# Optimization experiments

Measured on AMD Instinct MI355X. Metric: run time of the kernel, lower is better.

The kernel has to match this reference:

```python
import jax, jax.numpy as jnp
import numpy as np

IN_C, OUT_C = 32, 32
M1 = M2 = M3 = 12
CFT_M1 = CFT_M2 = M1 // 4  # 3
L_SEG, M_CHEB = 8, 6


def cft2d(x, m1, m2, L, M):
    # Piecewise Chebyshev projection along H (L segments, M polys), rFFT along W.
    # x: [N, C, H, W] -> complex [N, C, m1, m2]
    N, C, H, W = x.shape
    seg = H // L
    t = jnp.linspace(-1.0, 1.0, seg)
    theta = jnp.arccos(jnp.clip(t, -1.0, 1.0))
    P = jnp.cos(jnp.arange(M)[:, None] * theta[None, :])  # [M, seg] Chebyshev T_k
    xs = x.reshape(N, C, L, seg, W)
    coef = jnp.einsum('nclsw,ms->nclmw', xs, P) / seg      # [N,C,L,M,W]
    coef = coef.reshape(N, C, L * M, W)[:, :, :m1, :]      # keep first m1 coeffs
    return jnp.fft.rfft(coef, axis=-1)[:, :, :, :m2]       # [N,C,m1,m2] complex


def setup_inputs() -> dict:
    key = jax.random.key(0)
    ks = jax.random.split(key, 16)
    B, H, W, D = 4, 64, 64, 64
    scale = 1.0 / (IN_C * OUT_C)
    wshape = (IN_C, OUT_C, M1, M2, M3)
    inp = {'x': jax.random.normal(ks[0], (B, IN_C, H, W, D), dtype=jnp.float32)}
    for i in range(4):
        inp[f'w{i+1}_re'] = scale * jax.random.uniform(ks[1 + 2 * i], wshape, dtype=jnp.float32)
        inp[f'w{i+1}_im'] = scale * jax.random.uniform(ks[2 + 2 * i], wshape, dtype=jnp.float32)
    cft_flat = IN_C * CFT_M1 * CFT_M2 * 2  # 576
    hidden = (IN_C + OUT_C) * 2            # 128
    inp['mlp_w1'] = 0.02 * jax.random.normal(ks[9], (cft_flat, hidden), dtype=jnp.float32)
    inp['mlp_b1'] = jnp.zeros((hidden,), dtype=jnp.float32)
    inp['mlp_w2'] = 0.02 * jax.random.normal(ks[10], (hidden, OUT_C), dtype=jnp.float32)
    inp['mlp_b2'] = jnp.zeros((OUT_C,), dtype=jnp.float32)
    inp['corr_scale'] = jnp.float32(0.1)
    return inp


def reference(x, w1_re, w1_im, w2_re, w2_im, w3_re, w3_im, w4_re, w4_im,
              mlp_w1, mlp_b1, mlp_w2, mlp_b2, corr_scale):
    B, C, H, W, D = x.shape
    O = mlp_w2.shape[1]
    x_ft = jnp.fft.rfftn(x, axes=(-3, -2, -1))  # [B,C,H,W,D//2+1] complex64

    def mix(xb, wre, wim):
        return jnp.einsum('bixyz,ioxyz->boxyz', xb, wre + 1j * wim)

    out_ft = jnp.zeros((B, O, H, W, D // 2 + 1), dtype=x_ft.dtype)
    out_ft = out_ft.at[:, :, :M1, :M2, :M3].set(mix(x_ft[:, :, :M1, :M2, :M3], w1_re, w1_im))
    out_ft = out_ft.at[:, :, -M1:, :M2, :M3].set(mix(x_ft[:, :, -M1:, :M2, :M3], w2_re, w2_im))
    out_ft = out_ft.at[:, :, :M1, -M2:, :M3].set(mix(x_ft[:, :, :M1, -M2:, :M3], w3_re, w3_im))
    out_ft = out_ft.at[:, :, -M1:, -M2:, :M3].set(mix(x_ft[:, :, -M1:, -M2:, :M3], w4_re, w4_im))
    x_fno = jnp.fft.irfftn(out_ft, s=(H, W, D), axes=(-3, -2, -1))

    # Chebyshev-Fourier correction branch over depth slices
    xs = jnp.transpose(x, (0, 4, 1, 2, 3)).reshape(B * D, C, H, W)
    cft = cft2d(xs, CFT_M1, CFT_M2, L_SEG, M_CHEB)                 # [B*D,C,3,3] complex
    cft_flat = jnp.stack([cft.real, cft.imag], axis=-1).reshape(B * D, -1)  # view_as_real order
    h = jax.nn.gelu(cft_flat @ mlp_w1 + mlp_b1, approximate=False)
    corr = h @ mlp_w2 + mlp_b2                                     # [B*D, O]
    corr = jnp.transpose(corr.reshape(B, D, O), (0, 2, 1))[:, :, None, None, :]  # [B,O,1,1,D]
    return x_fno + corr_scale * corr
```

## Files before the change

### kernel.cpp

```cpp
#include <hip/hip_runtime.h>
#include <math.h>


#define CMUL_STEP(t, u) do { float _nx = (t).x*(u).x - (t).y*(u).y; \
    (t).y = (t).x*(u).y + (t).y*(u).x; (t).x = _nx; } while (0)

constexpr float TW_C[64] = {
     1.000000000000000f,  0.995184726672197f,  0.980785280403230f,  0.956940335732209f,
     0.923879532511287f,  0.881921264348355f,  0.831469612302545f,  0.773010453362737f,
     0.707106781186548f,  0.634393284163645f,  0.555570233019602f,  0.471396736825998f,
     0.382683432365090f,  0.290284677254462f,  0.195090322016128f,  0.098017140329561f,
     0.000000000000000f, -0.098017140329561f, -0.195090322016128f, -0.290284677254462f,
    -0.382683432365090f, -0.471396736825998f, -0.555570233019602f, -0.634393284163645f,
    -0.707106781186548f, -0.773010453362737f, -0.831469612302545f, -0.881921264348355f,
    -0.923879532511287f, -0.956940335732209f, -0.980785280403230f, -0.995184726672197f,
    -1.000000000000000f, -0.995184726672197f, -0.980785280403230f, -0.956940335732209f,
    -0.923879532511287f, -0.881921264348355f, -0.831469612302545f, -0.773010453362737f,
    -0.707106781186548f, -0.634393284163645f, -0.555570233019602f, -0.471396736825998f,
    -0.382683432365090f, -0.290284677254462f, -0.195090322016128f, -0.098017140329561f,
     0.000000000000000f,  0.098017140329561f,  0.195090322016128f,  0.290284677254462f,
     0.382683432365090f,  0.471396736825998f,  0.555570233019602f,  0.634393284163645f,
     0.707106781186548f,  0.773010453362737f,  0.831469612302545f,  0.881921264348355f,
     0.923879532511287f,  0.956940335732209f,  0.980785280403230f,  0.995184726672197f
};
constexpr float twc(int m) { return TW_C[m & 63]; }
constexpr float tws(int m) { return TW_C[(m + 48) & 63]; }

static __device__ __forceinline__ void fill_tw(float2* tw, int tid, int nthr) {
    for (int m = tid; m < 64; m += nthr) {
        float s, c;
        sincosf((float)m * 0.09817477042468103f, &s, &c);
        tw[m] = make_float2(c, s);
    }
}

static __device__ __forceinline__ void ystage_pair(const float2* __restrict__ Ar,
                                                   const float2* __restrict__ Br,
                                                   int ap, float2& A, float2& Bc) {
    const float2 zw0 = Ar[0];
    const float2 zw32 = Ar[32];
    const float sg = (ap & 1) ? -1.f : 1.f;
    A.x = zw0.x + sg * zw32.x;  A.y = zw0.y + sg * zw32.y;
    Bc = A;
    float s_, c_;
    sincosf((float)ap * 0.09817477042468103f, &s_, &c_);
    const float2 u = make_float2(c_, s_);
    float2 t = u;
    {
        float2 za = Ar[1], zb = Br[1];
        float Ex = za.x + zb.x, Ey = za.y + zb.y;
        float Ox = za.x - zb.x, Oy = za.y - zb.y;
        A.x  += t.x * Ex + t.y * Oy;  A.y  += t.x * Ey - t.y * Ox;
        Bc.x += t.x * Ex - t.y * Oy;  Bc.y += t.x * Ey + t.y * Ox;
    }
    #pragma unroll
    for (int w = 2; w < 32; w += 2) {
        CMUL_STEP(t, u);
        const float4 a4 = *(const float4*)(Ar + w);
        const float4 b4 = *(const float4*)(Br + w);
        {
            float Ex = a4.x + b4.x, Ey = a4.y + b4.y;
            float Ox = a4.x - b4.x, Oy = a4.y - b4.y;
            A.x  += t.x * Ex + t.y * Oy;  A.y  += t.x * Ey - t.y * Ox;
            Bc.x += t.x * Ex - t.y * Oy;  Bc.y += t.x * Ey + t.y * Ox;
        }
        CMUL_STEP(t, u);
        {
            float Ex = a4.z + b4.z, Ey = a4.w + b4.w;
            float Ox = a4.z - b4.z, Oy = a4.w - b4.w;
            A.x  += t.x * Ex + t.y * Oy;  A.y  += t.x * Ey - t.y * Ox;
            Bc.x += t.x * Ex - t.y * Oy;  Bc.y += t.x * Ey + t.y * Ox;
        }
    }
}

template<int KZ0>
static __device__ __forceinline__ void zstage_wave(const float* __restrict__ row,
                                                   float2* __restrict__ zA,
                                                   float2* __restrict__ zB,
                                                   int w) {
    float a0x, a0y = 0.f, a1x, a1y = 0.f, a2x, a2y = 0.f;
#define ACCD(dd, xa, xb) do { \
    const float e_ = (xa) + (xb), o_ = (xa) - (xb); \
    a0x += e_ * twc((KZ0    ) * (dd));  a0y -= o_ * tws((KZ0    ) * (dd)); \
    a1x += e_ * twc((KZ0 + 1) * (dd));  a1y -= o_ * tws((KZ0 + 1) * (dd)); \
    a2x += e_ * twc((KZ0 + 2) * (dd));  a2y -= o_ * tws((KZ0 + 2) * (dd)); } while (0)
    float4 qa  = *(const float4*)(row + 0);
    float4 qm1 = *(const float4*)(row + 60);
    float4 qm0 = *(const float4*)(row + 56);
    const float x0v = qa.x;
    a0x = x0v; a1x = x0v; a2x = x0v;
    ACCD(1, qa.y, qm1.w);
    ACCD(2, qa.z, qm1.z);
    ACCD(3, qa.w, qm1.y);
    float mnext = qm1.x;
    qa = *(const float4*)(row + 4);
    ACCD(4, qa.x, mnext);
    ACCD(5, qa.y, qm0.w);
    ACCD(6, qa.z, qm0.z);
    ACCD(7, qa.w, qm0.y);
    mnext = qm0.x;
    qm0 = *(const float4*)(row + 52);
    qa  = *(const float4*)(row + 8);
    ACCD(8,  qa.x, mnext);
    ACCD(9,  qa.y, qm0.w);
    ACCD(10, qa.z, qm0.z);
    ACCD(11, qa.w, qm0.y);
    mnext = qm0.x;
    qm0 = *(const float4*)(row + 48);
    qa  = *(const float4*)(row + 12);
    ACCD(12, qa.x, mnext);
    ACCD(13, qa.y, qm0.w);
    ACCD(14, qa.z, qm0.z);
    ACCD(15, qa.w, qm0.y);
    mnext = qm0.x;
    qm0 = *(const float4*)(row + 44);
    qa  = *(const float4*)(row + 16);
    ACCD(16, qa.x, mnext);
    ACCD(17, qa.y, qm0.w);
    ACCD(18, qa.z, qm0.z);
    ACCD(19, qa.w, qm0.y);
    mnext = qm0.x;
    qm0 = *(const float4*)(row + 40);
    qa  = *(const float4*)(row + 20);
    ACCD(20, qa.x, mnext);
    ACCD(21, qa.y, qm0.w);
    ACCD(22, qa.z, qm0.z);
    ACCD(23, qa.w, qm0.y);
    mnext = qm0.x;
    qm0 = *(const float4*)(row + 36);
    qa  = *(const float4*)(row + 24);
    ACCD(24, qa.x, mnext);
    ACCD(25, qa.y, qm0.w);
    ACCD(26, qa.z, qm0.z);
    ACCD(27, qa.w, qm0.y);
    mnext = qm0.x;
    qm0 = *(const float4*)(row + 32);
    qa  = *(const float4*)(row + 28);
    ACCD(28, qa.x, mnext);
    ACCD(29, qa.y, qm0.w);
    ACCD(30, qa.z, qm0.z);
    ACCD(31, qa.w, qm0.y);
    const float x32v = qm0.x;
#undef ACCD
    const float s0 = ((KZ0     & 1)) ? -x32v : x32v;
    const float s1 = (((KZ0+1) & 1)) ? -x32v : x32v;
    a0x += s0; a1x += s1; a2x += s0;
    zA[(KZ0    ) * 66 + w] = make_float2(a0x, a0y);
    zA[(KZ0 + 1) * 66 + w] = make_float2(a1x, a1y);
    zA[(KZ0 + 2) * 66 + w] = make_float2(a2x, a2y);
    const int wm = 64 - w;
    zB[(KZ0    ) * 66 + wm] = make_float2(a0x, a0y);
    zB[(KZ0 + 1) * 66 + wm] = make_float2(a1x, a1y);
    zB[(KZ0 + 2) * 66 + wm] = make_float2(a2x, a2y);
}

__global__ __launch_bounds__(256) void k_fwd_zy(const float* __restrict__ x,
                                                float2* __restrict__ X2) {
    __shared__ __align__(16) float xt[64 * 68];
    __shared__ __align__(16) float2 zA[12 * 66];
    __shared__ __align__(16) float2 zB[12 * 66];
    const int tid = threadIdx.x;
    const int blk = blockIdx.x;
    const float4* xrow4 = (const float4*)(x + (size_t)blk * 4096);
    for (int r = 0; r < 4; ++r) {
        int i4 = r * 256 + tid;
        int w = i4 >> 4, d4 = (i4 & 15) << 2;
        *(float4*)&xt[w * 68 + d4] = xrow4[i4];
    }
    __syncthreads();
    {
        const int q = tid >> 6, w = tid & 63;
        const float* row = &xt[w * 68];
        switch (q) {
            case 0: zstage_wave<0>(row, zA, zB, w); break;
            case 1: zstage_wave<3>(row, zA, zB, w); break;
            case 2: zstage_wave<6>(row, zA, zB, w); break;
            default: zstage_wave<9>(row, zA, zB, w); break;
        }
    }
    __syncthreads();
    float2* xout = X2 + (size_t)blk * 288;
    if (tid < 156) {
        const int ap = tid / 12, kz = tid - (tid / 12) * 12;
        float2 A, Bc;
        ystage_pair(&zA[kz * 66], &zB[kz * 66], ap, A, Bc);
        if (ap <= 11) xout[ap * 12 + kz] = A;
        if (ap >= 1)  xout[(24 - ap) * 12 + kz] = Bc;
    }
}

__global__ __launch_bounds__(256) void k_fwd_x(const float2* __restrict__ X2,
                                               float2* __restrict__ X3) {
    __shared__ __align__(16) float2 s2A[12 * 66];
    __shared__ __align__(16) float2 s2B[12 * 66];
    const int tid = threadIdx.x;
    const int blk = blockIdx.x;
    const int ay = blk % 24, bc = blk / 24;
    const float2* src = X2 + (size_t)bc * (64 * 288) + ay * 12;
    for (int i4 = tid; i4 < 384; i4 += 256) {
        int hh = i4 / 6, c4 = i4 - hh * 6;
        float4 v = ((const float4*)(src + (size_t)hh * 288))[c4];
        int kz = 2 * c4;
        s2A[kz * 66 + hh]            = make_float2(v.x, v.y);
        s2A[(kz + 1) * 66 + hh]      = make_float2(v.z, v.w);
        s2B[kz * 66 + (64 - hh)]     = make_float2(v.x, v.y);
        s2B[(kz + 1) * 66 + (64 - hh)] = make_float2(v.z, v.w);
    }
    __syncthreads();
    float2* dst = X3 + (size_t)bc * 6912 + ay * 12;
    if (tid < 156) {
        const int ap = tid / 12, kz = tid - (tid / 12) * 12;
        float2 A, Bc;
        ystage_pair(&s2A[kz * 66], &s2B[kz * 66], ap, A, Bc);
        if (ap <= 11) dst[ap * 288 + kz] = A;
        if (ap >= 1)  dst[(24 - ap) * 288 + kz] = Bc;
    }
}

__global__ __launch_bounds__(384) void k_mix(const float2* __restrict__ X3,
                                             float2* __restrict__ F,
        const float* __restrict__ w1re, const float* __restrict__ w1im,
        const float* __restrict__ w2re, const float* __restrict__ w2im,
        const float* __restrict__ w3re, const float* __restrict__ w3im,
        const float* __restrict__ w4re, const float* __restrict__ w4im) {
    __shared__ float2 xs[128 * 12];
    const int tid = threadIdx.x;
    const int blk = blockIdx.x;
    const int ax = blk / 24, ay = blk % 24;
    const int cx = ax >= 12 ? 1 : 0, cy = ay >= 12 ? 1 : 0;
    const int m1 = ax - cx * 12, m2 = ay - cy * 12;
    const int sel = cx + cy * 2;
    const float* wre = sel == 0 ? w1re : sel == 1 ? w2re : sel == 2 ? w3re : w4re;
    const float* wim = sel == 0 ? w1im : sel == 1 ? w2im : sel == 2 ? w3im : w4im;
    const size_t moff = (size_t)ax * 288 + (size_t)ay * 12;
    for (int i = tid; i < 1536; i += 384) {
        int bi = i / 12, kz = i - bi * 12;
        xs[i] = X3[(size_t)bi * 6912 + moff + kz];
    }
    __syncthreads();
    const int o = tid / 12, kz = tid - (tid / 12) * 12;
    const int wbase = o * 1728 + m1 * 144 + m2 * 12 + kz;
    float2 A0 = make_float2(0.f, 0.f), A1 = A0, A2 = A0, A3 = A0;
    for (int i = 0; i < 32; ++i) {
        float wr = wre[i * 55296 + wbase];
        float wi = wim[i * 55296 + wbase];
        float2 x0 = xs[i * 12 + kz];
        float2 x1 = xs[(32 + i) * 12 + kz];
        float2 x2 = xs[(64 + i) * 12 + kz];
        float2 x3 = xs[(96 + i) * 12 + kz];
        A0.x += x0.x * wr - x0.y * wi; A0.y += x0.x * wi + x0.y * wr;
        A1.x += x1.x * wr - x1.y * wi; A1.y += x1.x * wi + x1.y * wr;
        A2.x += x2.x * wr - x2.y * wi; A2.y += x2.x * wi + x2.y * wr;
        A3.x += x3.x * wr - x3.y * wi; A3.y += x3.x * wi + x3.y * wr;
    }
    F[(size_t)(0 * 32 + o) * 6912 + moff + kz] = A0;
    F[(size_t)(1 * 32 + o) * 6912 + moff + kz] = A1;
    F[(size_t)(2 * 32 + o) * 6912 + moff + kz] = A2;
    F[(size_t)(3 * 32 + o) * 6912 + moff + kz] = A3;
}

__global__ __launch_bounds__(256) void k_inv_x(const float2* __restrict__ F,
                                               float2* __restrict__ Y1) {
    __shared__ __align__(16) float2 fs[24 * 12];
    __shared__ float2 tw[64];
    const int tid = threadIdx.x;
    const int blk = blockIdx.x;
    const int ay = blk % 24, bo = blk / 24;
    fill_tw(tw, tid, 256);
    const float2* src = F + (size_t)bo * 6912 + ay * 12;
    for (int i4 = tid; i4 < 144; i4 += 256) {
        int ax = i4 / 6, c4 = i4 - ax * 6;
        ((float4*)&fs[ax * 12])[c4] = ((const float4*)(src + (size_t)ax * 288))[c4];
    }
    __syncthreads();
    float2* dst = Y1 + (size_t)bo * (64 * 288) + ay * 12;
    for (int idx = tid; idx < 396; idx += 256) {
        int hp = idx / 12, kz = idx - (idx / 12) * 12;
        float2 f0  = fs[kz];
        float2 f12 = fs[12 * 12 + kz];
        float2 t12 = tw[(52 * hp) & 63];
        float2 A, Bc;
        A.x  = f0.x + f12.x * t12.x - f12.y * t12.y;
        A.y  = f0.y + f12.x * t12.y + f12.y * t12.x;
        Bc.x = f0.x + f12.x * t12.x + f12.y * t12.y;
        Bc.y = f0.y + f12.y * t12.x - f12.x * t12.y;
        const float2 u = tw[hp];
        float2 t = u;
        for (int a = 1; a <= 11; ++a) {
            float2 fa = fs[a * 12 + kz];
            float2 fb = fs[(24 - a) * 12 + kz];
            float Ex = fa.x + fb.x, Ey = fa.y + fb.y;
            float Ox = fa.x - fb.x, Oy = fa.y - fb.y;
            A.x  += t.x * Ex - t.y * Oy;  A.y  += t.x * Ey + t.y * Ox;
            Bc.x += t.x * Ex + t.y * Oy;  Bc.y += t.x * Ey - t.y * Ox;
            CMUL_STEP(t, u);
        }
        dst[hp * 288 + kz] = A;
        if (hp >= 1 && hp <= 31) dst[(64 - hp) * 288 + kz] = Bc;
    }
}

__global__ __launch_bounds__(256) void k_cft(const float* __restrict__ x,
                                             float* __restrict__ cft) {
    __shared__ float2 tw[64];
    __shared__ float red[3 * 64 * 18];
    const int tid = threadIdx.x;
    const int blk = blockIdx.x;
    const int d = tid & 63, q = tid >> 6;
    fill_tw(tw, tid, 256);
    __syncthreads();
    float aR[3][3] = {{0.f}}, aI[3][3] = {{0.f}};
    const float* xb = x + (size_t)blk * 262144;
    for (int wi = 0; wi < 16; ++wi) {
        const int w = q * 16 + wi;
        float c0 = 0.f, c1 = 0.f, c2 = 0.f;
        #pragma unroll
        for (int s = 0; s < 8; ++s) {
            float xv = xb[(size_t)(s * 64 + w) * 64 + d];
            float t = (2.0f * (float)s - 7.0f) * (1.0f / 7.0f);
            c0 += xv;
            c1 += xv * t;
            c2 += xv * (2.0f * t * t - 1.0f);
        }
        c0 *= 0.125f; c1 *= 0.125f; c2 *= 0.125f;
        #pragma unroll
        for (int f = 0; f < 3; ++f) {
            float2 t = tw[(f * w) & 63];
            aR[0][f] += c0 * t.x; aI[0][f] -= c0 * t.y;
            aR[1][f] += c1 * t.x; aI[1][f] -= c1 * t.y;
            aR[2][f] += c2 * t.x; aI[2][f] -= c2 * t.y;
        }
    }
    if (q > 0) {
        float* dst = &red[((q - 1) * 64 + d) * 18];
        #pragma unroll
        for (int k = 0; k < 3; ++k)
            #pragma unroll
            for (int f = 0; f < 3; ++f) {
                dst[k * 6 + f * 2]     = aR[k][f];
                dst[k * 6 + f * 2 + 1] = aI[k][f];
            }
    }
    __syncthreads();
    if (q == 0) {
        #pragma unroll
        for (int qq = 0; qq < 3; ++qq) {
            const float* sr = &red[(qq * 64 + d) * 18];
            #pragma unroll
            for (int k = 0; k < 3; ++k)
                #pragma unroll
                for (int f = 0; f < 3; ++f) {
                    aR[k][f] += sr[k * 6 + f * 2];
                    aI[k][f] += sr[k * 6 + f * 2 + 1];
                }
        }
        const int b = blk >> 5, c = blk & 31;
        float* dst = cft + (size_t)(b * 64 + d) * 576 + c * 18;
        #pragma unroll
        for (int k = 0; k < 3; ++k)
            #pragma unroll
            for (int f = 0; f < 3; ++f) {
                dst[k * 6 + f * 2]     = aR[k][f];
                dst[k * 6 + f * 2 + 1] = aI[k][f];
            }
    }
}

__global__ __launch_bounds__(128) void k_mlp(const float* __restrict__ cft,
                                             const float* __restrict__ w1,
                                             const float* __restrict__ b1,
                                             const float* __restrict__ w2,
                                             const float* __restrict__ b2,
                                             const float* __restrict__ cs,
                                             float* __restrict__ corr) {
    __shared__ float row[576];
    __shared__ float hbuf[128];
    const int n = blockIdx.x;
    const int tid = threadIdx.x;
    for (int i = tid; i < 576; i += 128) row[i] = cft[(size_t)n * 576 + i];
    __syncthreads();
    float acc = b1[tid];
    #pragma unroll 8
    for (int k = 0; k < 576; ++k) acc += row[k] * w1[k * 128 + tid];
    hbuf[tid] = 0.5f * acc * (1.0f + erff(acc * 0.70710678118654752f));
    __syncthreads();
    if (tid < 32) {
        float a2 = b2[tid];
        #pragma unroll 8
        for (int k = 0; k < 128; ++k) a2 += hbuf[k] * w2[k * 32 + tid];
        const int b = n >> 6, d = n & 63;
        corr[(b * 32 + tid) * 64 + d] = a2 * cs[0];
    }
}

__global__ __launch_bounds__(256) void k_inv_yz(const float2* __restrict__ Y1,
                                                const float* __restrict__ corr,
                                                float* __restrict__ out) {
    __shared__ __align__(16) float2 y1[288];
    __shared__ __align__(16) float2 y2[64 * 12];
    __shared__ float2 tw[64];
    __shared__ float corrl[64];
    const int tid = threadIdx.x;
    const int blk = blockIdx.x;
    const int bo = blk >> 6;
    fill_tw(tw, tid, 256);
    {
        const float4* src4 = (const float4*)(Y1 + (size_t)blk * 288);
        for (int i4 = tid; i4 < 144; i4 += 256) ((float4*)y1)[i4] = src4[i4];
    }
    if (tid < 64) corrl[tid] = corr[bo * 64 + tid];
    __syncthreads();
    {
        const int w = tid >> 2, kz0 = (tid & 3) * 3;
        float2 a0 = make_float2(0.f, 0.f), a1 = a0, a2 = a0;
        {
            float2 f0 = y1[kz0], f1 = y1[kz0 + 1], f2 = y1[kz0 + 2];
            a0.x += f0.x; a0.y += f0.y;
            a1.x += f1.x; a1.y += f1.y;
            a2.x += f2.x; a2.y += f2.y;
        }
        {
            float2 t = tw[(52 * w) & 63];
            float2 f0 = y1[144 + kz0], f1 = y1[144 + kz0 + 1], f2 = y1[144 + kz0 + 2];
            a0.x += f0.x * t.x - f0.y * t.y; a0.y += f0.x * t.y + f0.y * t.x;
            a1.x += f1.x * t.x - f1.y * t.y; a1.y += f1.x * t.y + f1.y * t.x;
            a2.x += f2.x * t.x - f2.y * t.y; a2.y += f2.x * t.y + f2.y * t.x;
        }
        const float2 u = tw[w];
        float2 t = u;
        for (int a = 1; a <= 11; ++a) {
            const float2* fa = &y1[a * 12 + kz0];
            const float2* fb = &y1[(24 - a) * 12 + kz0];
            float2 p0 = fa[0], p1 = fa[1], p2 = fa[2];
            float2 q0 = fb[0], q1 = fb[1], q2 = fb[2];
            float Ex, Ey, Ox, Oy;
            Ex = p0.x + q0.x; Ey = p0.y + q0.y; Ox = p0.x - q0.x; Oy = p0.y - q0.y;
            a0.x += t.x * Ex - t.y * Oy; a0.y += t.x * Ey + t.y * Ox;
            Ex = p1.x + q1.x; Ey = p1.y + q1.y; Ox = p1.x - q1.x; Oy = p1.y - q1.y;
            a1.x += t.x * Ex - t.y * Oy; a1.y += t.x * Ey + t.y * Ox;
            Ex = p2.x + q2.x; Ey = p2.y + q2.y; Ox = p2.x - q2.x; Oy = p2.y - q2.y;
            a2.x += t.x * Ex - t.y * Oy; a2.y += t.x * Ey + t.y * Ox;
            CMUL_STEP(t, u);
        }
        y2[w * 12 + kz0]     = a0;
        y2[w * 12 + kz0 + 1] = a1;
        y2[w * 12 + kz0 + 2] = a2;
    }
    float ctw[12], stw[12];
    const int d = tid & 63;
    #pragma unroll
    for (int kz = 0; kz < 12; ++kz) {
        float2 t = tw[(kz * d) & 63];
        float sc = (kz == 0 ? 1.0f : 2.0f) * (1.0f / 262144.0f);
        ctw[kz] = t.x * sc;
        stw[kz] = t.y * sc;
    }
    __syncthreads();
    const float cv = corrl[d];
    float* orow = out + (size_t)blk * 4096;
    const int wq = tid >> 6;
    for (int r = 0; r < 16; ++r) {
        int w = r * 4 + wq;
        const float4* yv = (const float4*)&y2[w * 12];
        float4 p0 = yv[0], p1 = yv[1], p2 = yv[2];
        float4 p3 = yv[3], p4 = yv[4], p5 = yv[5];
        float s = cv;
        s += p0.x * ctw[0]  - p0.y * stw[0];
        s += p0.z * ctw[1]  - p0.w * stw[1];
        s += p1.x * ctw[2]  - p1.y * stw[2];
        s += p1.z * ctw[3]  - p1.w * stw[3];
        s += p2.x * ctw[4]  - p2.y * stw[4];
        s += p2.z * ctw[5]  - p2.w * stw[5];
        s += p3.x * ctw[6]  - p3.y * stw[6];
        s += p3.z * ctw[7]  - p3.w * stw[7];
        s += p4.x * ctw[8]  - p4.y * stw[8];
        s += p4.z * ctw[9]  - p4.w * stw[9];
        s += p5.x * ctw[10] - p5.y * stw[10];
        s += p5.z * ctw[11] - p5.w * stw[11];
        orow[w * 64 + d] = s;
    }
}

extern "C" void kernel_launch(void* const* d_in, const int* in_sizes, int n_in,
                              void* d_out, int out_size, void* d_ws, size_t ws_size,
                              hipStream_t stream) {
    const float* x    = (const float*)d_in[0];
    const float* w1re = (const float*)d_in[1];
    const float* w1im = (const float*)d_in[2];
    const float* w2re = (const float*)d_in[3];
    const float* w2im = (const float*)d_in[4];
    const float* w3re = (const float*)d_in[5];
    const float* w3im = (const float*)d_in[6];
    const float* w4re = (const float*)d_in[7];
    const float* w4im = (const float*)d_in[8];
    const float* mw1  = (const float*)d_in[9];
    const float* mb1  = (const float*)d_in[10];
    const float* mw2  = (const float*)d_in[11];
    const float* mb2  = (const float*)d_in[12];
    const float* cs   = (const float*)d_in[13];
    float* out = (float*)d_out;

    char* ws = (char*)d_ws;
    float2* X2   = (float2*)(ws);
    float2* X3   = (float2*)(ws + 18874368);
    float2* F    = (float2*)(ws + 25952256);
    float*  cft  = (float*) (ws + 33030144);
    float*  corr = (float*) (ws + 33619968);
    float2* Y1   = X2;

    hipLaunchKernelGGL(k_fwd_zy, dim3(8192), dim3(256), 0, stream, x, X2);
    hipLaunchKernelGGL(k_fwd_x,  dim3(3072), dim3(256), 0, stream, X2, X3);
    hipLaunchKernelGGL(k_mix,    dim3(576),  dim3(384), 0, stream, X3, F,
                       w1re, w1im, w2re, w2im, w3re, w3im, w4re, w4im);
    hipLaunchKernelGGL(k_inv_x,  dim3(3072), dim3(256), 0, stream, F, Y1);
    hipLaunchKernelGGL(k_cft,    dim3(128),  dim3(256), 0, stream, x, cft);
    hipLaunchKernelGGL(k_mlp,    dim3(256),  dim3(128), 0, stream,
                       cft, mw1, mb1, mw2, mb2, cs, corr);
    hipLaunchKernelGGL(k_inv_yz, dim3(8192), dim3(256), 0, stream, Y1, corr, out);
}
```

Measured before the change: 479.7 us.

## Use one wave per block in z-stage FFT, loading rows into registers

The forward z/y stage now launches 64-thread blocks. Each thread loads its whole 64-element row straight into registers and computes all 12 z-modes itself, so the shared-memory staging of x and its barrier are gone. The y-stage work is looped over the single wave instead of being spread across 256 threads. This trades four-wave parallelism per block for fewer LDS round trips, at the cost of higher register pressure (64 loaded floats plus 24 accumulators) and more serial work per thread.

```diff
diff --git a/kernel.cpp b/kernel.cpp
--- a/kernel.cpp
+++ b/kernel.cpp
@@ -74,119 +74,57 @@
     }
 }
 
-template<int KZ0>
-static __device__ __forceinline__ void zstage_wave(const float* __restrict__ row,
-                                                   float2* __restrict__ zA,
-                                                   float2* __restrict__ zB,
-                                                   int w) {
-    float a0x, a0y = 0.f, a1x, a1y = 0.f, a2x, a2y = 0.f;
-#define ACCD(dd, xa, xb) do { \
-    const float e_ = (xa) + (xb), o_ = (xa) - (xb); \
-    a0x += e_ * twc((KZ0    ) * (dd));  a0y -= o_ * tws((KZ0    ) * (dd)); \
-    a1x += e_ * twc((KZ0 + 1) * (dd));  a1y -= o_ * tws((KZ0 + 1) * (dd)); \
-    a2x += e_ * twc((KZ0 + 2) * (dd));  a2y -= o_ * tws((KZ0 + 2) * (dd)); } while (0)
-    float4 qa  = *(const float4*)(row + 0);
-    float4 qm1 = *(const float4*)(row + 60);
-    float4 qm0 = *(const float4*)(row + 56);
-    const float x0v = qa.x;
-    a0x = x0v; a1x = x0v; a2x = x0v;
-    ACCD(1, qa.y, qm1.w);
-    ACCD(2, qa.z, qm1.z);
-    ACCD(3, qa.w, qm1.y);
-    float mnext = qm1.x;
-    qa = *(const float4*)(row + 4);
-    ACCD(4, qa.x, mnext);
-    ACCD(5, qa.y, qm0.w);
-    ACCD(6, qa.z, qm0.z);
-    ACCD(7, qa.w, qm0.y);
-    mnext = qm0.x;
-    qm0 = *(const float4*)(row + 52);
-    qa  = *(const float4*)(row + 8);
-    ACCD(8,  qa.x, mnext);
-    ACCD(9,  qa.y, qm0.w);
-    ACCD(10, qa.z, qm0.z);
-    ACCD(11, qa.w, qm0.y);
-    mnext = qm0.x;
-    qm0 = *(const float4*)(row + 48);
-    qa  = *(const float4*)(row + 12);
-    ACCD(12, qa.x, mnext);
-    ACCD(13, qa.y, qm0.w);
-    ACCD(14, qa.z, qm0.z);
-    ACCD(15, qa.w, qm0.y);
-    mnext = qm0.x;
-    qm0 = *(const float4*)(row + 44);
-    qa  = *(const float4*)(row + 16);
-    ACCD(16, qa.x, mnext);
-    ACCD(17, qa.y, qm0.w);
-    ACCD(18, qa.z, qm0.z);
-    ACCD(19, qa.w, qm0.y);
-    mnext = qm0.x;
-    qm0 = *(const float4*)(row + 40);
-    qa  = *(const float4*)(row + 20);
-    ACCD(20, qa.x, mnext);
-    ACCD(21, qa.y, qm0.w);
-    ACCD(22, qa.z, qm0.z);
-    ACCD(23, qa.w, qm0.y);
-    mnext = qm0.x;
-    qm0 = *(const float4*)(row + 36);
-    qa  = *(const float4*)(row + 24);
-    ACCD(24, qa.x, mnext);
-    ACCD(25, qa.y, qm0.w);
-    ACCD(26, qa.z, qm0.z);
-    ACCD(27, qa.w, qm0.y);
-    mnext = qm0.x;
-    qm0 = *(const float4*)(row + 32);
-    qa  = *(const float4*)(row + 28);
-    ACCD(28, qa.x, mnext);
-    ACCD(29, qa.y, qm0.w);
-    ACCD(30, qa.z, qm0.z);
-    ACCD(31, qa.w, qm0.y);
-    const float x32v = qm0.x;
-#undef ACCD
-    const float s0 = ((KZ0     & 1)) ? -x32v : x32v;
-    const float s1 = (((KZ0+1) & 1)) ? -x32v : x32v;
-    a0x += s0; a1x += s1; a2x += s0;
-    zA[(KZ0    ) * 66 + w] = make_float2(a0x, a0y);
-    zA[(KZ0 + 1) * 66 + w] = make_float2(a1x, a1y);
-    zA[(KZ0 + 2) * 66 + w] = make_float2(a2x, a2y);
-    const int wm = 64 - w;
-    zB[(KZ0    ) * 66 + wm] = make_float2(a0x, a0y);
-    zB[(KZ0 + 1) * 66 + wm] = make_float2(a1x, a1y);
-    zB[(KZ0 + 2) * 66 + wm] = make_float2(a2x, a2y);
-}
-
-__global__ __launch_bounds__(256) void k_fwd_zy(const float* __restrict__ x,
-                                                float2* __restrict__ X2) {
-    __shared__ __align__(16) float xt[64 * 68];
+__global__ __launch_bounds__(64) void k_fwd_zy(const float* __restrict__ x,
+                                               float2* __restrict__ X2) {
     __shared__ __align__(16) float2 zA[12 * 66];
     __shared__ __align__(16) float2 zB[12 * 66];
-    const int tid = threadIdx.x;
-    const int blk = blockIdx.x;
-    const float4* xrow4 = (const float4*)(x + (size_t)blk * 4096);
-    for (int r = 0; r < 4; ++r) {
-        int i4 = r * 256 + tid;
-        int w = i4 >> 4, d4 = (i4 & 15) << 2;
-        *(float4*)&xt[w * 68 + d4] = xrow4[i4];
-    }
-    __syncthreads();
+    const int w = threadIdx.x;
+    const int blk = blockIdx.x;
+    const float4* row4 = (const float4*)(x + (size_t)blk * 4096 + (size_t)w * 64);
+    float4 q[16];
+    #pragma unroll
+    for (int j = 0; j < 16; ++j) q[j] = row4[j];
+    float ax[12], ay[12];
     {
-        const int q = tid >> 6, w = tid & 63;
-        const float* row = &xt[w * 68];
-        switch (q) {
-            case 0: zstage_wave<0>(row, zA, zB, w); break;
-            case 1: zstage_wave<3>(row, zA, zB, w); break;
-            case 2: zstage_wave<6>(row, zA, zB, w); break;
-            default: zstage_wave<9>(row, zA, zB, w); break;
-        }
+        const float x0v = q[0].x, x32v = q[8].x;
+        #pragma unroll
+        for (int k = 0; k < 12; ++k) {
+            ax[k] = x0v + ((k & 1) ? -x32v : x32v);
+            ay[k] = 0.f;
+        }
+    }
+#define QE(dd) ((dd) & 3) == 0 ? q[(dd) >> 2].x : ((dd) & 3) == 1 ? q[(dd) >> 2].y : \
+               ((dd) & 3) == 2 ? q[(dd) >> 2].z : q[(dd) >> 2].w
+    #pragma unroll
+    for (int d = 1; d < 32; ++d) {
+        const float xa = QE(d);
+        const float xb = QE(64 - d);
+        const float e = xa + xb, o = xa - xb;
+        #pragma unroll
+        for (int k = 0; k < 12; ++k) {
+            ax[k] += e * twc(k * d);
+            ay[k] -= o * tws(k * d);
+        }
+    }
+#undef QE
+    #pragma unroll
+    for (int k = 0; k < 12; ++k) {
+        float2 v = make_float2(ax[k], ay[k]);
+        zA[k * 66 + w] = v;
+        zB[k * 66 + (64 - w)] = v;
     }
     __syncthreads();
     float2* xout = X2 + (size_t)blk * 288;
-    if (tid < 156) {
-        const int ap = tid / 12, kz = tid - (tid / 12) * 12;
-        float2 A, Bc;
-        ystage_pair(&zA[kz * 66], &zB[kz * 66], ap, A, Bc);
-        if (ap <= 11) xout[ap * 12 + kz] = A;
-        if (ap >= 1)  xout[(24 - ap) * 12 + kz] = Bc;
+    #pragma unroll
+    for (int base = 0; base < 156; base += 64) {
+        const int item = base + w;
+        if (item < 156) {
+            const int ap = item / 12, kz = item - (item / 12) * 12;
+            float2 A, Bc;
+            ystage_pair(&zA[kz * 66], &zB[kz * 66], ap, A, Bc);
+            if (ap <= 11) xout[ap * 12 + kz] = A;
+            if (ap >= 1)  xout[(24 - ap) * 12 + kz] = Bc;
+        }
     }
 }
 
@@ -509,7 +447,7 @@
     float*  corr = (float*) (ws + 33619968);
     float2* Y1   = X2;
 
-    hipLaunchKernelGGL(k_fwd_zy, dim3(8192), dim3(256), 0, stream, x, X2);
+    hipLaunchKernelGGL(k_fwd_zy, dim3(8192), dim3(64),  0, stream, x, X2);
     hipLaunchKernelGGL(k_fwd_x,  dim3(3072), dim3(256), 0, stream, X2, X3);
     hipLaunchKernelGGL(k_mix,    dim3(576),  dim3(384), 0, stream, X3, F,
                        w1re, w1im, w2re, w2im, w3re, w3im, w4re, w4im);
```

After: 449.7 us. -6.3%, faster.
